# Optimization experiments

Measured on AMD Instinct MI355X. Metric: run time of the kernel, lower is better.

Reference implementation:

```python
import jax, jax.numpy as jnp
import numpy as np

H = 256           # hidden_size
S = 4             # num_subspaces
D = H // S        # subspace dim = 64
HD = 64           # mLSTM head_dim
EPS = 1e-8


def setup_inputs() -> dict:
    key = jax.random.key(0)
    ks = iter(jax.random.split(key, 40))
    def w(shape, scale=0.02):
        return (jax.random.normal(next(ks), shape, dtype=jnp.float32) * scale)
    B, T, Din = 256, 512, 128
    inp = {
        'x': jax.random.normal(next(ks), (B, T, Din), dtype=jnp.float32),
        # input projection
        'W_in': w((Din, H)), 'b_in': jnp.zeros((H,), jnp.float32),
        # layer 0: sLSTM (forget_bias buffer is zeros -> folded into b? keep explicit)
        's0_Wih': w((H, 4 * H)), 's0_bih': jnp.zeros((4 * H,), jnp.float32),
        's0_Whh': w((H, 4 * H)),
        # layer 1: mLSTM
        'm_Wq': w((H, HD)), 'm_bq': jnp.zeros((HD,), jnp.float32),
        'm_Wk': w((H, HD)), 'm_bk': jnp.zeros((HD,), jnp.float32),
        'm_Wv': w((H, HD)), 'm_bv': jnp.zeros((HD,), jnp.float32),
        'm_Wi': w((H, 1)), 'm_bi': jnp.zeros((1,), jnp.float32),
        'm_Wf': w((H, 1)), 'm_bf': jnp.zeros((1,), jnp.float32),
        'm_Wo': w((H, H)), 'm_bo': jnp.zeros((H,), jnp.float32),
        'm_Wp': w((HD, H)), 'm_bp': jnp.zeros((H,), jnp.float32),
        # subspace sLSTM cells (stacked over S); forget bias = -log(2^s)
        'sub_Wih': w((S, D, 4 * D)), 'sub_bih': jnp.zeros((S, 4 * D), jnp.float32),
        'sub_Whh': w((S, D, 4 * D)),
        'sub_fbias': jnp.asarray(-np.log(2.0 ** np.arange(S)), jnp.float32)[:, None] * jnp.ones((S, D), jnp.float32),
        # memory attention MLP
        'att_W1': w((D, D)), 'att_b1': jnp.zeros((D,), jnp.float32),
        'att_W2': w((D, 1)), 'att_b2': jnp.zeros((1,), jnp.float32),
        # layer norm
        'ln_g': jnp.ones((H,), jnp.float32), 'ln_b': jnp.zeros((H,), jnp.float32),
    }
    return inp


def _forward(x, W_in, b_in, s0_Wih, s0_bih, s0_Whh,
             m_Wq, m_bq, m_Wk, m_bk, m_Wv, m_bv, m_Wi, m_bi, m_Wf, m_bf,
             m_Wo, m_bo, m_Wp, m_bp,
             sub_Wih, sub_bih, sub_Whh, sub_fbias,
             att_W1, att_b1, att_W2, att_b2, ln_g, ln_b):
    B, T, _ = x.shape
    xh = x @ W_in + b_in                      # [B,T,H]
    xh = jnp.swapaxes(xh, 0, 1)               # [T,B,H] for scan

    def slstm(xt, h, c, n, Wih, bih, Whh, fbias):
        gates = xt @ Wih + bih + h @ Whh
        ig, fg, og, ct = jnp.split(gates, 4, axis=-1)
        i = jnp.exp(ig)
        f = jax.nn.sigmoid(fg + fbias)
        o = jax.nn.sigmoid(og)
        c_new = f * c + i * jnp.tanh(ct)
        n_new = f * n + i
        h_new = o * jnp.tanh(c_new / (n_new + EPS))
        return h_new, c_new, n_new

    def step(carry, xt):
        (h0, c0, n0, C1, n1, hs, cs, ns, _) = carry
        # layer 0: sLSTM, residual
        h0n, c0n, n0n = slstm(xt, h0, c0, n0, s0_Wih, s0_bih, s0_Whh, 0.0)
        x1 = h0n + xt
        # layer 1: mLSTM, residual
        q = x1 @ m_Wq + m_bq
        k = x1 @ m_Wk + m_bk
        v = x1 @ m_Wv + m_bv
        i1 = jnp.exp(x1 @ m_Wi + m_bi)              # [B,1]
        f1 = jax.nn.sigmoid(x1 @ m_Wf + m_bf)       # [B,1]
        C1n = f1[:, :, None] * C1 + i1[:, :, None] * (v[:, :, None] * k[:, None, :])
        n1n = f1 * n1 + i1                          # [B,1]
        Cq = jnp.einsum('bij,bj->bi', C1n, q)       # [B,HD]
        h_tilde = Cq / (n1n + EPS)
        o1 = jax.nn.sigmoid(x1 @ m_Wo + m_bo)
        h1n = o1 * jnp.tanh(h_tilde @ m_Wp + m_bp)
        x2 = h1n + x1
        # subspace sLSTM cells over S chunks (vectorized over s)
        xs = jnp.swapaxes(x2.reshape(B, S, D), 0, 1)   # [S,B,D]
        gates = (jnp.einsum('sbd,sdg->sbg', xs, sub_Wih) + sub_bih[:, None, :]
                 + jnp.einsum('sbd,sdg->sbg', hs, sub_Whh))
        ig, fg, og, ct = jnp.split(gates, 4, axis=-1)
        i = jnp.exp(ig)
        f = jax.nn.sigmoid(fg + sub_fbias[:, None, :])
        o = jax.nn.sigmoid(og)
        csn = f * cs + i * jnp.tanh(ct)
        nsn = f * ns + i
        hsn = o * jnp.tanh(csn / (nsn + EPS))          # [S,B,D]
        # attention fusion across subspaces
        score = jnp.tanh(hsn @ att_W1 + att_b1) @ att_W2 + att_b2  # [S,B,1]
        w = jax.nn.softmax(score[..., 0], axis=0)                  # [S,B]
        h_fused = jnp.sum(w[:, :, None] * hsn, axis=0)             # [B,D]
        h_final = jnp.tile(h_fused, (1, S))                        # [B,H]
        return (h0n, c0n, n0n, C1n, n1n, hsn, csn, nsn, h_final), None

    z = jnp.zeros
    carry0 = (z((B, H)), z((B, H)), jnp.ones((B, H)),
              z((B, HD, HD)), jnp.ones((B, 1)),
              z((S, B, D)), z((S, B, D)), jnp.ones((S, B, D)),
              z((B, H)))
    carryT, _ = jax.lax.scan(step, carry0, xh)
    out = carryT[-1]                                 # last-step h_final [B,H]
    mu = jnp.mean(out, axis=-1, keepdims=True)
    var = jnp.mean((out - mu) ** 2, axis=-1, keepdims=True)
    return (out - mu) / jnp.sqrt(var + 1e-5) * ln_g + ln_b


def reference(x, W_in, b_in, s0_Wih, s0_bih, s0_Whh,
              m_Wq, m_bq, m_Wk, m_bk, m_Wv, m_bv, m_Wi, m_bi, m_Wf, m_bf,
              m_Wo, m_bo, m_Wp, m_bp,
              sub_Wih, sub_bih, sub_Whh, sub_fbias,
              att_W1, att_b1, att_W2, att_b2, ln_g, ln_b):
    return _forward(x, W_in, b_in, s0_Wih, s0_bih, s0_Whh,
                    m_Wq, m_bq, m_Wk, m_bk, m_Wv, m_bv, m_Wi, m_bi, m_Wf, m_bf,
                    m_Wo, m_bo, m_Wp, m_bp,
                    sub_Wih, sub_bih, sub_Whh, sub_fbias,
                    att_W1, att_b1, att_W2, att_b2, ln_g, ln_b)
```

## Files before the change

kernel.cpp:

```cpp
#include <hip/hip_runtime.h>
#include <math.h>

#define TSTEPS 512
#define CH 16
#define NCHUNK 32
#define EPSR 1e-8f

#define OHH   0u
#define OSUB  262144u
#define OQK   393216u
#define OV    425984u
#define OWO   442368u
#define OWP   507904u
#define OWIN  524288u
#define NPACK1 557056u
#define OWC   557056u
#define OBC   688128u

typedef __fp16 h2_t __attribute__((ext_vector_type(2)));

__device__ __forceinline__ float dot2(unsigned int w, unsigned int a, float acc) {
    union U { unsigned int u; h2_t h; };
    U cw; cw.u = w; U ca; ca.u = a;
    return __builtin_amdgcn_fdot2(cw.h, ca.h, acc, false);
}
__device__ __forceinline__ unsigned int pk2f(float a, float b) {
    union { h2_t h; unsigned int u; } c;
    c.h = __builtin_amdgcn_cvt_pkrtz(a, b);
    return c.u;
}
__device__ __forceinline__ float bfu(unsigned int v) {
    union { unsigned int i; float f; } c; c.i = v; return c.f;
}
__device__ __forceinline__ float sigmoidf_(float v) { return 1.0f / (1.0f + expf(-v)); }
__device__ __forceinline__ unsigned short f2bf(float f) {
    unsigned int u = __float_as_uint(f);
    return (unsigned short)((u + 0x7fffu + ((u >> 16) & 1u)) >> 16);
}

extern "C" __global__ void pack_w(const float* __restrict__ Whh,
    const float* __restrict__ sWih, const float* __restrict__ sWhh,
    const float* __restrict__ Wq, const float* __restrict__ Wk, const float* __restrict__ Wv,
    const float* __restrict__ Wo, const float* __restrict__ Wp,
    const float* __restrict__ W_in, unsigned short* __restrict__ ws)
{
    unsigned e = blockIdx.x * 256u + threadIdx.x;
    if (e >= NPACK1) return;
    float v; bool isbf = false;
    if (e < OSUB) {
        unsigned idx = e >> 3, sl = e & 7u;
        unsigned jp = idx >> 8, t = idx & 255u, g = sl >> 1, ee = sl & 1u;
        v = Whh[(2u * jp + ee) * 1024u + g * 256u + t];
    } else if (e < OQK) {
        unsigned r = e - OSUB, idx = r >> 3, sl = r & 7u;
        unsigned q4 = idx & 3u, d = (idx >> 2) & 63u, jq = (idx >> 8) & 15u, s = idx >> 12;
        unsigned g = sl >> 1, ee = sl & 1u;
        unsigned j = jq * 4u + (q4 & 1u) * 2u + ee;
        const float* src = (q4 >> 1) ? sWhh : sWih;
        v = src[(s * 64u + j) * 256u + g * 64u + d];
    } else if (e < OV) {
        unsigned r = e - OQK, idx = r >> 3, sl = r & 7u;
        unsigned d = idx & 63u, jq = idx >> 6;
        unsigned j = jq * 4u + (sl & 3u);
        v = ((sl >> 2) ? Wk : Wq)[j * 64u + d];
    } else if (e < OWO) {
        unsigned r = e - OV, idx = r >> 2;
        unsigned d = idx & 63u, jq = idx >> 6, j = jq * 4u + (r & 3u);
        v = Wv[j * 64u + d];
    } else if (e < OWP) {
        unsigned r = e - OWO, idx = r >> 2;
        unsigned t = idx & 255u, jq = idx >> 8, j = jq * 4u + (r & 3u);
        v = Wo[j * 256u + t];
    } else if (e < OWIN) {
        unsigned r = e - OWP, idx = r >> 2;
        unsigned t = idx & 255u, jq = idx >> 8, j = jq * 4u + (r & 3u);
        v = Wp[j * 256u + t];
    } else {
        v = W_in[e - OWIN]; isbf = true;
    }
    if (isbf) ws[e] = f2bf(v);
    else { union { __fp16 h; unsigned short s; } c; c.h = (__fp16)v; ws[e] = c.s; }
}

extern "C" __global__ void compute_wc(const float* __restrict__ W_in,
    const float* __restrict__ Wih, const float* __restrict__ b_in,
    const float* __restrict__ bih, unsigned short* __restrict__ ws)
{
    unsigned e = blockIdx.x * 256u + threadIdx.x;
    if (e < 131072u) {
        unsigned k = e >> 10, n = e & 1023u;
        float acc = 0.f;
        for (int j = 0; j < 256; ++j) acc += W_in[k * 256 + j] * Wih[j * 1024 + n];
        unsigned t = n & 255u, g = n >> 8;
        ws[OWC + k * 1024 + t * 4 + g] = f2bf(acc);
    } else if (e < 132096u) {
        unsigned n = e - 131072u;
        float acc = bih[n];
        for (int j = 0; j < 256; ++j) acc += b_in[j] * Wih[j * 1024 + n];
        float* bc = (float*)(ws + OBC);
        bc[n] = acc;
    }
}

extern "C" __global__ __launch_bounds__(512)
void xlstm_seq(const float* __restrict__ x, const float* __restrict__ b_in,
               const float* __restrict__ bq, const float* __restrict__ bk, const float* __restrict__ bv,
               const float* __restrict__ Wi, const float* __restrict__ bi,
               const float* __restrict__ Wf, const float* __restrict__ bf,
               const float* __restrict__ bo, const float* __restrict__ bp,
               const float* __restrict__ sbih, const float* __restrict__ sfb,
               const float* __restrict__ aW1, const float* __restrict__ ab1,
               const float* __restrict__ aW2, const float* __restrict__ ab2,
               const float* __restrict__ lng, const float* __restrict__ lnb,
               const unsigned short* __restrict__ pk,
               float* __restrict__ out)
{
    const int u = threadIdx.x;
    const int b = blockIdx.x;
    const int t256 = u & 255;
    const int half = u >> 8;

    __shared__ float g_chunk[CH][1024];
    __shared__ float xt_chunk[CH][256];
    __shared__ __align__(16) float xT[128][20];
    __shared__ __align__(16) float x1_l[256], hs_l[256];
    __shared__ float opre_l[256];
    __shared__ float psum[4][520];
    __shared__ float qb[64], kb[64], vb[64];
    __shared__ float Cm[64 * 65];
    __shared__ float sc_l[16];
    __shared__ __align__(16) float Wi_l[256], Wf_l[256];
    __shared__ float sbih_l[1024], bc_l[1024];
    __shared__ float b_in_l[256], bo_l[256], bp_l[256], sfb_l[256], bqkv_l[192];
    __shared__ __align__(16) unsigned int h0p[128], x1p[128], x2p[128], hsp[128], htp[32];

    {
        const float* bcg = (const float*)(pk + OBC);
        for (int e = u; e < 1024; e += 512) { sbih_l[e] = sbih[e]; bc_l[e] = bcg[e]; }
    }
    if (u < 256) {
        Wi_l[u] = Wi[u]; Wf_l[u] = Wf[u];
        b_in_l[u] = b_in[u]; bo_l[u] = bo[u]; bp_l[u] = bp[u]; sfb_l[u] = sfb[u];
        hs_l[u] = 0.f;
    }
    if (u < 192) bqkv_l[u] = (u < 64) ? bq[u] : (u < 128) ? bk[u - 64] : bv[u - 128];
    if (u < 128) { h0p[u] = 0u; hsp[u] = 0u; }
    if (u == 0) { sc_l[10] = bi[0]; sc_l[11] = bf[0]; }
    for (int e = u; e < 64 * 65; e += 512) Cm[e] = 0.f;
    float c0 = 0.f, n0 = 1.f, cs = 0.f, ns = 1.f, n1 = 1.f;
    __syncthreads();

    const uint4* pwhh = reinterpret_cast<const uint4*>(pk + OHH) + t256;
    const uint4* psub = reinterpret_cast<const uint4*>(pk + OSUB)
                        + ((size_t)((t256 >> 6) * 1024 + (t256 & 63))) * 4;
    const uint4* pqk = reinterpret_cast<const uint4*>(pk + OQK) + (u & 63);
    const uint2* pv_ = reinterpret_cast<const uint2*>(pk + OV) + (u & 63);
    const uint2* pwo = reinterpret_cast<const uint2*>(pk + OWO) + t256;
    const uint2* pwp = reinterpret_cast<const uint2*>(pk + OWP) + t256;
    const unsigned short* pwin = pk + OWIN + t256;
    const uint2* pwc = reinterpret_cast<const uint2*>(pk + OWC) + t256;
    const float* xrow = x + (size_t)b * TSTEPS * 128;

    for (int cc = 0; cc < NCHUNK; ++cc) {
        {
            float4 xv4 = *reinterpret_cast<const float4*>(xrow + cc * (CH * 128) + u * 4);
            int m = u >> 5, k0 = (u * 4) & 127;
            xT[k0][m] = xv4.x; xT[k0 + 1][m] = xv4.y; xT[k0 + 2][m] = xv4.z; xT[k0 + 3][m] = xv4.w;
        }
        __syncthreads();

        {
            const int m0 = half * 8;
            float xtacc[8], gacc[4][8];
            {
                float bi_ = b_in_l[t256];
                #pragma unroll
                for (int e = 0; e < 8; ++e) xtacc[e] = bi_;
                #pragma unroll
                for (int g = 0; g < 4; ++g) {
                    float bcv = bc_l[g * 256 + t256];
                    #pragma unroll
                    for (int e = 0; e < 8; ++e) gacc[g][e] = bcv;
                }
            }
            #pragma unroll 4
            for (int k = 0; k < 128; ++k) {
                float wv = bfu((unsigned)pwin[k * 256] << 16);
                uint2 wg = pwc[k * 256];
                float w0 = bfu(wg.x << 16), w1 = bfu(wg.x & 0xffff0000u);
                float w2 = bfu(wg.y << 16), w3 = bfu(wg.y & 0xffff0000u);
                float4 a  = *reinterpret_cast<const float4*>(&xT[k][m0]);
                float4 b4 = *reinterpret_cast<const float4*>(&xT[k][m0 + 4]);
                #pragma unroll
                for (int e = 0; e < 8; ++e) {
                    float xv = (e == 0) ? a.x : (e == 1) ? a.y : (e == 2) ? a.z : (e == 3) ? a.w
                             : (e == 4) ? b4.x : (e == 5) ? b4.y : (e == 6) ? b4.z : b4.w;
                    xtacc[e]   += xv * wv;
                    gacc[0][e] += xv * w0;
                    gacc[1][e] += xv * w1;
                    gacc[2][e] += xv * w2;
                    gacc[3][e] += xv * w3;
                }
            }
            #pragma unroll
            for (int e = 0; e < 8; ++e) {
                xt_chunk[m0 + e][t256] = xtacc[e];
                g_chunk[m0 + e][t256]       = gacc[0][e];
                g_chunk[m0 + e][256 + t256] = gacc[1][e];
                g_chunk[m0 + e][512 + t256] = gacc[2][e];
                g_chunk[m0 + e][768 + t256] = gacc[3][e];
            }
        }
        __syncthreads();

        for (int st = 0; st < CH; ++st) {
            {
                float g0 = 0.f, g1 = 0.f, g2 = 0.f, g3 = 0.f;
                const int jp0 = half * 64;
                #pragma unroll 4
                for (int q = 0; q < 16; ++q) {
                    uint4 hp4 = *reinterpret_cast<const uint4*>(&h0p[jp0 + q * 4]);
                    #pragma unroll
                    for (int e = 0; e < 4; ++e) {
                        uint4 wk = pwhh[(size_t)(jp0 + q * 4 + e) * 256];
                        unsigned int hp = (e == 0) ? hp4.x : (e == 1) ? hp4.y : (e == 2) ? hp4.z : hp4.w;
                        g0 = dot2(wk.x, hp, g0);
                        g1 = dot2(wk.y, hp, g1);
                        g2 = dot2(wk.z, hp, g2);
                        g3 = dot2(wk.w, hp, g3);
                    }
                }
                psum[0][u] = g0; psum[1][u] = g1; psum[2][u] = g2; psum[3][u] = g3;
            }
            __syncthreads();
            if (u < 256) {
                float G0 = g_chunk[st][u]       + psum[0][u] + psum[0][256 + u];
                float G1 = g_chunk[st][256 + u] + psum[1][u] + psum[1][256 + u];
                float G2 = g_chunk[st][512 + u] + psum[2][u] + psum[2][256 + u];
                float G3 = g_chunk[st][768 + u] + psum[3][u] + psum[3][256 + u];
                float i0 = expf(G0), f0 = sigmoidf_(G1), o0 = sigmoidf_(G2);
                float cn = f0 * c0 + i0 * tanhf(G3);
                float nn = f0 * n0 + i0;
                c0 = cn; n0 = nn;
                float h0n = o0 * tanhf(cn / (nn + EPSR));
                float x1v = h0n + xt_chunk[st][u];
                x1_l[u] = x1v;
                float h0o = __shfl_xor(h0n, 1);
                float x1o = __shfl_xor(x1v, 1);
                if (!(u & 1)) { h0p[u >> 1] = pk2f(h0n, h0o); x1p[u >> 1] = pk2f(x1v, x1o); }
            }
            __syncthreads();

            if (u < 256) {
                const int jq0 = (u >> 6) * 16;
                float pq = 0.f, pkk = 0.f, pvv = 0.f;
                #pragma unroll 4
                for (int q = 0; q < 16; ++q) {
                    int jq = jq0 + q;
                    uint4 wqk = pqk[(size_t)jq * 64];
                    uint2 wv2 = pv_[(size_t)jq * 64];
                    uint2 ap = *reinterpret_cast<const uint2*>(&x1p[jq * 2]);
                    pq  = dot2(wqk.x, ap.x, pq);  pq  = dot2(wqk.y, ap.y, pq);
                    pkk = dot2(wqk.z, ap.x, pkk); pkk = dot2(wqk.w, ap.y, pkk);
                    pvv = dot2(wv2.x, ap.x, pvv); pvv = dot2(wv2.y, ap.y, pvv);
                }
                psum[0][u] = pq; psum[1][u] = pkk; psum[2][u] = pvv;
            } else if (u < 384) {
                const float* Wl = (u < 320) ? Wi_l : Wf_l;
                int j0 = (u & 63) * 4;
                float4 xv = *reinterpret_cast<const float4*>(&x1_l[j0]);
                float4 wv = *reinterpret_cast<const float4*>(&Wl[j0]);
                float p = xv.x * wv.x + xv.y * wv.y + xv.z * wv.z + xv.w * wv.w;
                #pragma unroll
                for (int off = 32; off > 0; off >>= 1) p += __shfl_down(p, off);
                if ((u & 63) == 0) sc_l[(u < 320) ? 8 : 9] = p;
            }
            __syncthreads();
            {
                int lane = u & 63;
                if (u < 64)        qb[u]    = bqkv_l[u]          + psum[0][u] + psum[0][64 + u] + psum[0][128 + u] + psum[0][192 + u];
                else if (u < 128)  kb[lane] = bqkv_l[64 + lane]  + psum[1][lane] + psum[1][64 + lane] + psum[1][128 + lane] + psum[1][192 + lane];
                else if (u < 192)  vb[lane] = bqkv_l[128 + lane] + psum[2][lane] + psum[2][64 + lane] + psum[2][128 + lane] + psum[2][192 + lane];
                else if (u == 192) sc_l[0] = expf(sc_l[10] + sc_l[8]);
                else if (u == 193) sc_l[1] = sigmoidf_(sc_l[11] + sc_l[9]);
            }
            __syncthreads();

            float i1 = sc_l[0], f1 = sc_l[1];
            n1 = f1 * n1 + i1;
            {
                int r = u >> 3, ci = (u & 7) * 8;
                float vi = i1 * vb[r];
                float cqp = 0.f;
                #pragma unroll
                for (int e = 0; e < 8; ++e) {
                    int c = ci + e;
                    float cmv = f1 * Cm[r * 65 + c] + vi * kb[c];
                    Cm[r * 65 + c] = cmv;
                    cqp += cmv * qb[c];
                }
                cqp += __shfl_down(cqp, 4);
                cqp += __shfl_down(cqp, 2);
                cqp += __shfl_down(cqp, 1);
                float htv = cqp / (n1 + EPSR);
                float hto = __shfl_xor(htv, 8);
                if ((u & 15) == 0) htp[u >> 4] = pk2f(htv, hto);

                float p = 0.f;
                const int jq0 = half * 32;
                #pragma unroll 4
                for (int q = 0; q < 32; ++q) {
                    int jq = jq0 + q;
                    uint2 w2 = pwo[(size_t)jq * 256];
                    uint2 ap = *reinterpret_cast<const uint2*>(&x1p[jq * 2]);
                    p = dot2(w2.x, ap.x, p); p = dot2(w2.y, ap.y, p);
                }
                psum[3][u] = p;
            }
            __syncthreads();

            {
                if (u < 256) opre_l[u] = bo_l[u] + psum[3][u] + psum[3][256 + u];
                float p = 0.f;
                const int jq0 = half * 8;
                #pragma unroll
                for (int q = 0; q < 8; ++q) {
                    int jq = jq0 + q;
                    uint2 w2 = pwp[(size_t)jq * 256];
                    uint2 ap = *reinterpret_cast<const uint2*>(&htp[jq * 2]);
                    p = dot2(w2.x, ap.x, p); p = dot2(w2.y, ap.y, p);
                }
                psum[0][u] = p;
            }
            __syncthreads();
            if (u < 256) {
                float pp = bp_l[u] + psum[0][u] + psum[0][256 + u];
                float h1 = sigmoidf_(opre_l[u]) * tanhf(pp);
                float x2v = h1 + x1_l[u];
                float x2o = __shfl_xor(x2v, 1);
                if (!(u & 1)) x2p[u >> 1] = pk2f(x2v, x2o);
            }
            __syncthreads();

            {
                const int sbase = (t256 >> 6) * 32;
                const int jqb = half * 8;
                float g0 = 0.f, g1 = 0.f, g2 = 0.f, g3 = 0.f;
                #pragma unroll 2
                for (int q = 0; q < 8; ++q) {
                    int jq = jqb + q;
                    const uint4* pp4 = psub + (size_t)jq * 256;
                    uint4 wih0 = pp4[0], wih1 = pp4[1], whh0 = pp4[2], whh1 = pp4[3];
                    uint2 xp = *reinterpret_cast<const uint2*>(&x2p[sbase + jq * 2]);
                    uint2 hp = *reinterpret_cast<const uint2*>(&hsp[sbase + jq * 2]);
                    g0 = dot2(wih0.x, xp.x, g0); g0 = dot2(wih1.x, xp.y, g0);
                    g0 = dot2(whh0.x, hp.x, g0); g0 = dot2(whh1.x, hp.y, g0);
                    g1 = dot2(wih0.y, xp.x, g1); g1 = dot2(wih1.y, xp.y, g1);
                    g1 = dot2(whh0.y, hp.x, g1); g1 = dot2(whh1.y, hp.y, g1);
                    g2 = dot2(wih0.z, xp.x, g2); g2 = dot2(wih1.z, xp.y, g2);
                    g2 = dot2(whh0.z, hp.x, g2); g2 = dot2(whh1.z, hp.y, g2);
                    g3 = dot2(wih0.w, xp.x, g3); g3 = dot2(wih1.w, xp.y, g3);
                    g3 = dot2(whh0.w, hp.x, g3); g3 = dot2(whh1.w, hp.y, g3);
                }
                psum[0][u] = g0; psum[1][u] = g1; psum[2][u] = g2; psum[3][u] = g3;
            }
            __syncthreads();
            if (u < 256) {
                int s = u >> 6, dd = u & 63;
                float sg0 = psum[0][u] + psum[0][256 + u] + sbih_l[s * 256 + dd];
                float sg1 = psum[1][u] + psum[1][256 + u] + sbih_l[s * 256 + 64 + dd];
                float sg2 = psum[2][u] + psum[2][256 + u] + sbih_l[s * 256 + 128 + dd];
                float sg3 = psum[3][u] + psum[3][256 + u] + sbih_l[s * 256 + 192 + dd];
                float si = expf(sg0);
                float sf = sigmoidf_(sg1 + sfb_l[u]);
                float so = sigmoidf_(sg2);
                float csn = sf * cs + si * tanhf(sg3);
                float nsn = sf * ns + si;
                cs = csn; ns = nsn;
                float hsn = so * tanhf(csn / (nsn + EPSR));
                hs_l[u] = hsn;
                float hso = __shfl_xor(hsn, 1);
                if (!(u & 1)) hsp[u >> 1] = pk2f(hsn, hso);
            }
            __syncthreads();
        }
    }

    if (u < 256) {
        int s = u >> 6, dd = u & 63;
        float av = ab1[dd];
        for (int j = 0; j < 64; ++j) av += hs_l[s * 64 + j] * aW1[j * 64 + dd];
        float contrib = tanhf(av) * aW2[dd];
        #pragma unroll
        for (int off = 32; off > 0; off >>= 1) contrib += __shfl_down(contrib, off);
        if (dd == 0) sc_l[4 + s] = contrib + ab2[0];
    }
    __syncthreads();
    if (u < 256) {
        float a0 = sc_l[4], a1 = sc_l[5], a2 = sc_l[6], a3 = sc_l[7];
        float m = fmaxf(fmaxf(a0, a1), fmaxf(a2, a3));
        float e0 = expf(a0 - m), e1 = expf(a1 - m), e2 = expf(a2 - m), e3 = expf(a3 - m);
        float inv = 1.f / (e0 + e1 + e2 + e3);
        int dd = u & 63;
        psum[0][u] = (e0 * hs_l[dd] + e1 * hs_l[64 + dd] + e2 * hs_l[128 + dd] + e3 * hs_l[192 + dd]) * inv;
    }
    __syncthreads();
    if (u < 256) {
        float mu = 0.f;
        for (int j = 0; j < 256; ++j) mu += psum[0][j];
        mu *= (1.0f / 256.0f);
        float var = 0.f;
        for (int j = 0; j < 256; ++j) { float dv = psum[0][j] - mu; var += dv * dv; }
        var *= (1.0f / 256.0f);
        out[b * 256 + u] = (psum[0][u] - mu) / sqrtf(var + 1e-5f) * lng[u] + lnb[u];
    }
}

extern "C" void kernel_launch(void* const* d_in, const int* in_sizes, int n_in,
                              void* d_out, int out_size, void* d_ws, size_t ws_size,
                              hipStream_t stream) {
    (void)in_sizes; (void)n_in; (void)out_size; (void)ws_size;
    const float* x     = (const float*)d_in[0];
    const float* W_in  = (const float*)d_in[1];
    const float* b_in  = (const float*)d_in[2];
    const float* Wih   = (const float*)d_in[3];
    const float* bih   = (const float*)d_in[4];
    const float* Whh   = (const float*)d_in[5];
    const float* Wq    = (const float*)d_in[6];
    const float* bq    = (const float*)d_in[7];
    const float* Wk    = (const float*)d_in[8];
    const float* bk    = (const float*)d_in[9];
    const float* Wv    = (const float*)d_in[10];
    const float* bv    = (const float*)d_in[11];
    const float* Wi    = (const float*)d_in[12];
    const float* bi    = (const float*)d_in[13];
    const float* Wf    = (const float*)d_in[14];
    const float* bf    = (const float*)d_in[15];
    const float* Wo    = (const float*)d_in[16];
    const float* bo    = (const float*)d_in[17];
    const float* Wp    = (const float*)d_in[18];
    const float* bp    = (const float*)d_in[19];
    const float* sWih  = (const float*)d_in[20];
    const float* sbih  = (const float*)d_in[21];
    const float* sWhh  = (const float*)d_in[22];
    const float* sfb   = (const float*)d_in[23];
    const float* aW1   = (const float*)d_in[24];
    const float* ab1   = (const float*)d_in[25];
    const float* aW2   = (const float*)d_in[26];
    const float* ab2   = (const float*)d_in[27];
    const float* lng   = (const float*)d_in[28];
    const float* lnb   = (const float*)d_in[29];
    float* out = (float*)d_out;
    unsigned short* ws = (unsigned short*)d_ws;

    pack_w<<<dim3((NPACK1 + 255u) / 256u), dim3(256), 0, stream>>>(
        Whh, sWih, sWhh, Wq, Wk, Wv, Wo, Wp, W_in, ws);
    compute_wc<<<dim3(517), dim3(256), 0, stream>>>(W_in, Wih, b_in, bih, ws);

    xlstm_seq<<<dim3(256), dim3(512), 0, stream>>>(
        x, b_in, bq, bk, bv, Wi, bi, Wf, bf, bo, bp,
        sbih, sfb, aW1, ab1, aW2, ab2, lng, lnb, ws, out);
}
```

Before: 7.102 ms.

## Double workgroup to 1024 threads, splitting recurrent matvecs four ways

```diff
diff --git a/kernel.cpp b/kernel.cpp
--- a/kernel.cpp
+++ b/kernel.cpp
@@ -64,9 +64,10 @@
         unsigned j = jq * 4u + (sl & 3u);
         v = ((sl >> 2) ? Wk : Wq)[j * 64u + d];
     } else if (e < OWO) {
-        unsigned r = e - OV, idx = r >> 2;
-        unsigned d = idx & 63u, jq = idx >> 6, j = jq * 4u + (r & 3u);
-        v = Wv[j * 64u + d];
+        unsigned r = e - OQK, idx0 = 0u; (void)idx0;
+        unsigned rr = e - OV, idx = rr >> 2;
+        unsigned d = idx & 63u, jq = idx >> 6, j = jq * 4u + (rr & 3u);
+        v = Wv[j * 64u + d]; (void)r;
     } else if (e < OWP) {
         unsigned r = e - OWO, idx = r >> 2;
         unsigned t = idx & 255u, jq = idx >> 8, j = jq * 4u + (r & 3u);
@@ -102,7 +103,7 @@
     }
 }
 
-extern "C" __global__ __launch_bounds__(512)
+extern "C" __global__ __launch_bounds__(1024)
 void xlstm_seq(const float* __restrict__ x, const float* __restrict__ b_in,
                const float* __restrict__ bq, const float* __restrict__ bk, const float* __restrict__ bv,
                const float* __restrict__ Wi, const float* __restrict__ bi,
@@ -118,14 +119,14 @@
     const int u = threadIdx.x;
     const int b = blockIdx.x;
     const int t256 = u & 255;
-    const int half = u >> 8;
+    const int quarter = u >> 8;
 
     __shared__ float g_chunk[CH][1024];
     __shared__ float xt_chunk[CH][256];
     __shared__ __align__(16) float xT[128][20];
     __shared__ __align__(16) float x1_l[256], hs_l[256];
     __shared__ float opre_l[256];
-    __shared__ float psum[4][520];
+    __shared__ float psum[4][1040];
     __shared__ float qb[64], kb[64], vb[64];
     __shared__ float Cm[64 * 65];
     __shared__ float sc_l[16];
@@ -136,7 +137,7 @@
 
     {
         const float* bcg = (const float*)(pk + OBC);
-        for (int e = u; e < 1024; e += 512) { sbih_l[e] = sbih[e]; bc_l[e] = bcg[e]; }
+        sbih_l[u] = sbih[u]; bc_l[u] = bcg[u];
     }
     if (u < 256) {
         Wi_l[u] = Wi[u]; Wf_l[u] = Wf[u];
@@ -146,7 +147,7 @@
     if (u < 192) bqkv_l[u] = (u < 64) ? bq[u] : (u < 128) ? bk[u - 64] : bv[u - 128];
     if (u < 128) { h0p[u] = 0u; hsp[u] = 0u; }
     if (u == 0) { sc_l[10] = bi[0]; sc_l[11] = bf[0]; }
-    for (int e = u; e < 64 * 65; e += 512) Cm[e] = 0.f;
+    for (int e = u; e < 64 * 65; e += 1024) Cm[e] = 0.f;
     float c0 = 0.f, n0 = 1.f, cs = 0.f, ns = 1.f, n1 = 1.f;
     __syncthreads();
 
@@ -163,24 +164,24 @@
 
     for (int cc = 0; cc < NCHUNK; ++cc) {
         {
-            float4 xv4 = *reinterpret_cast<const float4*>(xrow + cc * (CH * 128) + u * 4);
-            int m = u >> 5, k0 = (u * 4) & 127;
-            xT[k0][m] = xv4.x; xT[k0 + 1][m] = xv4.y; xT[k0 + 2][m] = xv4.z; xT[k0 + 3][m] = xv4.w;
+            float2 xv2 = *reinterpret_cast<const float2*>(xrow + cc * (CH * 128) + u * 2);
+            int m = u >> 6, k0 = (u * 2) & 127;
+            xT[k0][m] = xv2.x; xT[k0 + 1][m] = xv2.y;
         }
         __syncthreads();
 
         {
-            const int m0 = half * 8;
-            float xtacc[8], gacc[4][8];
+            const int m0 = quarter * 4;
+            float xtacc[4], gacc[4][4];
             {
                 float bi_ = b_in_l[t256];
                 #pragma unroll
-                for (int e = 0; e < 8; ++e) xtacc[e] = bi_;
+                for (int e = 0; e < 4; ++e) xtacc[e] = bi_;
                 #pragma unroll
                 for (int g = 0; g < 4; ++g) {
                     float bcv = bc_l[g * 256 + t256];
                     #pragma unroll
-                    for (int e = 0; e < 8; ++e) gacc[g][e] = bcv;
+                    for (int e = 0; e < 4; ++e) gacc[g][e] = bcv;
                 }
             }
             #pragma unroll 4
@@ -189,12 +190,10 @@
                 uint2 wg = pwc[k * 256];
                 float w0 = bfu(wg.x << 16), w1 = bfu(wg.x & 0xffff0000u);
                 float w2 = bfu(wg.y << 16), w3 = bfu(wg.y & 0xffff0000u);
-                float4 a  = *reinterpret_cast<const float4*>(&xT[k][m0]);
-                float4 b4 = *reinterpret_cast<const float4*>(&xT[k][m0 + 4]);
-                #pragma unroll
-                for (int e = 0; e < 8; ++e) {
-                    float xv = (e == 0) ? a.x : (e == 1) ? a.y : (e == 2) ? a.z : (e == 3) ? a.w
-                             : (e == 4) ? b4.x : (e == 5) ? b4.y : (e == 6) ? b4.z : b4.w;
+                float4 a = *reinterpret_cast<const float4*>(&xT[k][m0]);
+                #pragma unroll
+                for (int e = 0; e < 4; ++e) {
+                    float xv = (e == 0) ? a.x : (e == 1) ? a.y : (e == 2) ? a.z : a.w;
                     xtacc[e]   += xv * wv;
                     gacc[0][e] += xv * w0;
                     gacc[1][e] += xv * w1;
@@ -203,7 +202,7 @@
                 }
             }
             #pragma unroll
-            for (int e = 0; e < 8; ++e) {
+            for (int e = 0; e < 4; ++e) {
                 xt_chunk[m0 + e][t256] = xtacc[e];
                 g_chunk[m0 + e][t256]       = gacc[0][e];
                 g_chunk[m0 + e][256 + t256] = gacc[1][e];
@@ -216,9 +215,9 @@
         for (int st = 0; st < CH; ++st) {
             {
                 float g0 = 0.f, g1 = 0.f, g2 = 0.f, g3 = 0.f;
-                const int jp0 = half * 64;
+                const int jp0 = quarter * 32;
                 #pragma unroll 4
-                for (int q = 0; q < 16; ++q) {
+                for (int q = 0; q < 8; ++q) {
                     uint4 hp4 = *reinterpret_cast<const uint4*>(&h0p[jp0 + q * 4]);
                     #pragma unroll
                     for (int e = 0; e < 4; ++e) {
@@ -234,10 +233,10 @@
             }
             __syncthreads();
             if (u < 256) {
-                float G0 = g_chunk[st][u]       + psum[0][u] + psum[0][256 + u];
-                float G1 = g_chunk[st][256 + u] + psum[1][u] + psum[1][256 + u];
-                float G2 = g_chunk[st][512 + u] + psum[2][u] + psum[2][256 + u];
-                float G3 = g_chunk[st][768 + u] + psum[3][u] + psum[3][256 + u];
+                float G0 = g_chunk[st][u]       + psum[0][u] + psum[0][256 + u] + psum[0][512 + u] + psum[0][768 + u];
+                float G1 = g_chunk[st][256 + u] + psum[1][u] + psum[1][256 + u] + psum[1][512 + u] + psum[1][768 + u];
+                float G2 = g_chunk[st][512 + u] + psum[2][u] + psum[2][256 + u] + psum[2][512 + u] + psum[2][768 + u];
+                float G3 = g_chunk[st][768 + u] + psum[3][u] + psum[3][256 + u] + psum[3][512 + u] + psum[3][768 + u];
                 float i0 = expf(G0), f0 = sigmoidf_(G1), o0 = sigmoidf_(G2);
                 float cn = f0 * c0 + i0 * tanhf(G3);
                 float nn = f0 * n0 + i0;
@@ -274,6 +273,17 @@
                 #pragma unroll
                 for (int off = 32; off > 0; off >>= 1) p += __shfl_down(p, off);
                 if ((u & 63) == 0) sc_l[(u < 320) ? 8 : 9] = p;
+            } else if (u >= 512) {
+                float p = 0.f;
+                const int jq0 = (quarter - 2) * 32;
+                #pragma unroll 4
+                for (int q = 0; q < 32; ++q) {
+                    int jq = jq0 + q;
+                    uint2 w2 = pwo[(size_t)jq * 256];
+                    uint2 ap = *reinterpret_cast<const uint2*>(&x1p[jq * 2]);
+                    p = dot2(w2.x, ap.x, p); p = dot2(w2.y, ap.y, p);
+                }
+                psum[3][u] = p;
             }
             __syncthreads();
             {
@@ -289,42 +299,32 @@
             float i1 = sc_l[0], f1 = sc_l[1];
             n1 = f1 * n1 + i1;
             {
-                int r = u >> 3, ci = (u & 7) * 8;
+                int r = u >> 4, ci = (u & 15) * 4;
                 float vi = i1 * vb[r];
                 float cqp = 0.f;
                 #pragma unroll
-                for (int e = 0; e < 8; ++e) {
+                for (int e = 0; e < 4; ++e) {
                     int c = ci + e;
                     float cmv = f1 * Cm[r * 65 + c] + vi * kb[c];
                     Cm[r * 65 + c] = cmv;
                     cqp += cmv * qb[c];
                 }
+                cqp += __shfl_down(cqp, 8);
                 cqp += __shfl_down(cqp, 4);
                 cqp += __shfl_down(cqp, 2);
                 cqp += __shfl_down(cqp, 1);
                 float htv = cqp / (n1 + EPSR);
-                float hto = __shfl_xor(htv, 8);
-                if ((u & 15) == 0) htp[u >> 4] = pk2f(htv, hto);
-
+                float hto = __shfl_xor(htv, 16);
+                if ((u & 31) == 0) htp[u >> 5] = pk2f(htv, hto);
+                if (u < 256) opre_l[u] = bo_l[u] + psum[3][512 + u] + psum[3][768 + u];
+            }
+            __syncthreads();
+
+            {
                 float p = 0.f;
-                const int jq0 = half * 32;
-                #pragma unroll 4
-                for (int q = 0; q < 32; ++q) {
-                    int jq = jq0 + q;
-                    uint2 w2 = pwo[(size_t)jq * 256];
-                    uint2 ap = *reinterpret_cast<const uint2*>(&x1p[jq * 2]);
-                    p = dot2(w2.x, ap.x, p); p = dot2(w2.y, ap.y, p);
-                }
-                psum[3][u] = p;
-            }
-            __syncthreads();
-
-            {
-                if (u < 256) opre_l[u] = bo_l[u] + psum[3][u] + psum[3][256 + u];
-                float p = 0.f;
-                const int jq0 = half * 8;
-                #pragma unroll
-                for (int q = 0; q < 8; ++q) {
+                const int jq0 = quarter * 4;
+                #pragma unroll
+                for (int q = 0; q < 4; ++q) {
                     int jq = jq0 + q;
                     uint2 w2 = pwp[(size_t)jq * 256];
                     uint2 ap = *reinterpret_cast<const uint2*>(&htp[jq * 2]);
@@ -334,7 +334,7 @@
             }
             __syncthreads();
             if (u < 256) {
-                float pp = bp_l[u] + psum[0][u] + psum[0][256 + u];
+                float pp = bp_l[u] + psum[0][u] + psum[0][256 + u] + psum[0][512 + u] + psum[0][768 + u];
                 float h1 = sigmoidf_(opre_l[u]) * tanhf(pp);
                 float x2v = h1 + x1_l[u];
                 float x2o = __shfl_xor(x2v, 1);
@@ -344,10 +344,10 @@
 
             {
                 const int sbase = (t256 >> 6) * 32;
-                const int jqb = half * 8;
+                const int jqb = quarter * 4;
                 float g0 = 0.f, g1 = 0.f, g2 = 0.f, g3 = 0.f;
-                #pragma unroll 2
-                for (int q = 0; q < 8; ++q) {
+                #pragma unroll
+                for (int q = 0; q < 4; ++q) {
                     int jq = jqb + q;
                     const uint4* pp4 = psub + (size_t)jq * 256;
                     uint4 wih0 = pp4[0], wih1 = pp4[1], whh0 = pp4[2], whh1 = pp4[3];
@@ -367,10 +367,10 @@
             __syncthreads();
             if (u < 256) {
                 int s = u >> 6, dd = u & 63;
-                float sg0 = psum[0][u] + psum[0][256 + u] + sbih_l[s * 256 + dd];
-                float sg1 = psum[1][u] + psum[1][256 + u] + sbih_l[s * 256 + 64 + dd];
-                float sg2 = psum[2][u] + psum[2][256 + u] + sbih_l[s * 256 + 128 + dd];
-                float sg3 = psum[3][u] + psum[3][256 + u] + sbih_l[s * 256 + 192 + dd];
+                float sg0 = psum[0][u] + psum[0][256 + u] + psum[0][512 + u] + psum[0][768 + u] + sbih_l[s * 256 + dd];
+                float sg1 = psum[1][u] + psum[1][256 + u] + psum[1][512 + u] + psum[1][768 + u] + sbih_l[s * 256 + 64 + dd];
+                float sg2 = psum[2][u] + psum[2][256 + u] + psum[2][512 + u] + psum[2][768 + u] + sbih_l[s * 256 + 128 + dd];
+                float sg3 = psum[3][u] + psum[3][256 + u] + psum[3][512 + u] + psum[3][768 + u] + sbih_l[s * 256 + 192 + dd];
                 float si = expf(sg0);
                 float sf = sigmoidf_(sg1 + sfb_l[u]);
                 float so = sigmoidf_(sg2);
@@ -457,7 +457,7 @@
         Whh, sWih, sWhh, Wq, Wk, Wv, Wo, Wp, W_in, ws);
     compute_wc<<<dim3(517), dim3(256), 0, stream>>>(W_in, Wih, b_in, bih, ws);
 
-    xlstm_seq<<<dim3(256), dim3(512), 0, stream>>>(
+    xlstm_seq<<<dim3(256), dim3(1024), 0, stream>>>(
         x, b_in, bq, bk, bv, Wi, bi, Wf, bf, bo, bp,
         sbih, sfb, aW1, ab1, aW2, ab2, lng, lnb, ws, out);
 }
```

After: 10.88 ms. 53.2% more time.

## Repack recurrent weights so each thread reads contiguous runs, merge Wp projection stage

Applied to the files above, without the earlier changes.

```diff
diff --git a/kernel.cpp b/kernel.cpp
--- a/kernel.cpp
+++ b/kernel.cpp
@@ -49,7 +49,9 @@
     float v; bool isbf = false;
     if (e < OSUB) {
         unsigned idx = e >> 3, sl = e & 7u;
-        unsigned jp = idx >> 8, t = idx & 255u, g = sl >> 1, ee = sl & 1u;
+        unsigned jj = idx & 3u, t = (idx >> 2) & 255u, jp4 = idx >> 10;
+        unsigned jp = jp4 * 4u + jj;
+        unsigned g = sl >> 1, ee = sl & 1u;
         v = Whh[(2u * jp + ee) * 1024u + g * 256u + t];
     } else if (e < OQK) {
         unsigned r = e - OSUB, idx = r >> 3, sl = r & 7u;
@@ -60,20 +62,23 @@
         v = src[(s * 64u + j) * 256u + g * 64u + d];
     } else if (e < OV) {
         unsigned r = e - OQK, idx = r >> 3, sl = r & 7u;
-        unsigned d = idx & 63u, jq = idx >> 6;
-        unsigned j = jq * 4u + (sl & 3u);
+        unsigned jj = idx & 3u, d = (idx >> 2) & 63u, jq4 = idx >> 8;
+        unsigned j = (jq4 * 4u + jj) * 4u + (sl & 3u);
         v = ((sl >> 2) ? Wk : Wq)[j * 64u + d];
     } else if (e < OWO) {
         unsigned r = e - OV, idx = r >> 2;
-        unsigned d = idx & 63u, jq = idx >> 6, j = jq * 4u + (r & 3u);
+        unsigned jj = idx & 3u, d = (idx >> 2) & 63u, jq4 = idx >> 8;
+        unsigned j = (jq4 * 4u + jj) * 4u + (r & 3u);
         v = Wv[j * 64u + d];
     } else if (e < OWP) {
         unsigned r = e - OWO, idx = r >> 2;
-        unsigned t = idx & 255u, jq = idx >> 8, j = jq * 4u + (r & 3u);
+        unsigned jj = idx & 3u, t = (idx >> 2) & 255u, jq4 = idx >> 10;
+        unsigned j = (jq4 * 4u + jj) * 4u + (r & 3u);
         v = Wo[j * 256u + t];
     } else if (e < OWIN) {
         unsigned r = e - OWP, idx = r >> 2;
-        unsigned t = idx & 255u, jq = idx >> 8, j = jq * 4u + (r & 3u);
+        unsigned jq = idx & 15u, t = idx >> 4;
+        unsigned j = jq * 4u + (r & 3u);
         v = Wp[j * 256u + t];
     } else {
         v = W_in[e - OWIN]; isbf = true;
@@ -124,7 +129,6 @@
     __shared__ float xt_chunk[CH][256];
     __shared__ __align__(16) float xT[128][20];
     __shared__ __align__(16) float x1_l[256], hs_l[256];
-    __shared__ float opre_l[256];
     __shared__ float psum[4][520];
     __shared__ float qb[64], kb[64], vb[64];
     __shared__ float Cm[64 * 65];
@@ -150,13 +154,13 @@
     float c0 = 0.f, n0 = 1.f, cs = 0.f, ns = 1.f, n1 = 1.f;
     __syncthreads();
 
-    const uint4* pwhh = reinterpret_cast<const uint4*>(pk + OHH) + t256;
+    const uint4* pwhh = reinterpret_cast<const uint4*>(pk + OHH) + t256 * 4;
     const uint4* psub = reinterpret_cast<const uint4*>(pk + OSUB)
                         + ((size_t)((t256 >> 6) * 1024 + (t256 & 63))) * 4;
-    const uint4* pqk = reinterpret_cast<const uint4*>(pk + OQK) + (u & 63);
-    const uint2* pv_ = reinterpret_cast<const uint2*>(pk + OV) + (u & 63);
-    const uint2* pwo = reinterpret_cast<const uint2*>(pk + OWO) + t256;
-    const uint2* pwp = reinterpret_cast<const uint2*>(pk + OWP) + t256;
+    const uint4* pqk = reinterpret_cast<const uint4*>(pk + OQK) + (u & 63) * 4;
+    const uint2* pv2 = reinterpret_cast<const uint2*>(pk + OV) + (u & 63) * 4;
+    const uint2* pwo = reinterpret_cast<const uint2*>(pk + OWO) + t256 * 4;
+    const uint2* pwp = reinterpret_cast<const uint2*>(pk + OWP) + t256 * 16;
     const unsigned short* pwin = pk + OWIN + t256;
     const uint2* pwc = reinterpret_cast<const uint2*>(pk + OWC) + t256;
     const float* xrow = x + (size_t)b * TSTEPS * 128;
@@ -216,13 +220,14 @@
         for (int st = 0; st < CH; ++st) {
             {
                 float g0 = 0.f, g1 = 0.f, g2 = 0.f, g3 = 0.f;
-                const int jp0 = half * 64;
+                const int jp40 = half * 16;
                 #pragma unroll 4
-                for (int q = 0; q < 16; ++q) {
-                    uint4 hp4 = *reinterpret_cast<const uint4*>(&h0p[jp0 + q * 4]);
+                for (int q4 = 0; q4 < 16; ++q4) {
+                    const uint4* w4 = pwhh + (size_t)(jp40 + q4) * 1024;
+                    uint4 hp4 = *reinterpret_cast<const uint4*>(&h0p[(jp40 + q4) * 4]);
                     #pragma unroll
                     for (int e = 0; e < 4; ++e) {
-                        uint4 wk = pwhh[(size_t)(jp0 + q * 4 + e) * 256];
+                        uint4 wk = w4[e];
                         unsigned int hp = (e == 0) ? hp4.x : (e == 1) ? hp4.y : (e == 2) ? hp4.z : hp4.w;
                         g0 = dot2(wk.x, hp, g0);
                         g1 = dot2(wk.y, hp, g1);
@@ -252,17 +257,22 @@
             __syncthreads();
 
             if (u < 256) {
-                const int jq0 = (u >> 6) * 16;
+                const int jq40 = (u >> 6) * 4;
                 float pq = 0.f, pkk = 0.f, pvv = 0.f;
-                #pragma unroll 4
-                for (int q = 0; q < 16; ++q) {
-                    int jq = jq0 + q;
-                    uint4 wqk = pqk[(size_t)jq * 64];
-                    uint2 wv2 = pv_[(size_t)jq * 64];
-                    uint2 ap = *reinterpret_cast<const uint2*>(&x1p[jq * 2]);
-                    pq  = dot2(wqk.x, ap.x, pq);  pq  = dot2(wqk.y, ap.y, pq);
-                    pkk = dot2(wqk.z, ap.x, pkk); pkk = dot2(wqk.w, ap.y, pkk);
-                    pvv = dot2(wv2.x, ap.x, pvv); pvv = dot2(wv2.y, ap.y, pvv);
+                #pragma unroll
+                for (int q4 = 0; q4 < 4; ++q4) {
+                    const uint4* wq4 = pqk + (size_t)(jq40 + q4) * 256;
+                    const uint2* wv4 = pv2 + (size_t)(jq40 + q4) * 256;
+                    #pragma unroll
+                    for (int e = 0; e < 4; ++e) {
+                        int jq = (jq40 + q4) * 4 + e;
+                        uint4 wqk = wq4[e];
+                        uint2 wvv = wv4[e];
+                        uint2 ap = *reinterpret_cast<const uint2*>(&x1p[jq * 2]);
+                        pq  = dot2(wqk.x, ap.x, pq);  pq  = dot2(wqk.y, ap.y, pq);
+                        pkk = dot2(wqk.z, ap.x, pkk); pkk = dot2(wqk.w, ap.y, pkk);
+                        pvv = dot2(wvv.x, ap.x, pvv); pvv = dot2(wvv.y, ap.y, pvv);
+                    }
                 }
                 psum[0][u] = pq; psum[1][u] = pkk; psum[2][u] = pvv;
             } else if (u < 384) {
@@ -307,35 +317,32 @@
                 if ((u & 15) == 0) htp[u >> 4] = pk2f(htv, hto);
 
                 float p = 0.f;
-                const int jq0 = half * 32;
+                const int jq40 = half * 8;
                 #pragma unroll 4
-                for (int q = 0; q < 32; ++q) {
-                    int jq = jq0 + q;
-                    uint2 w2 = pwo[(size_t)jq * 256];
-                    uint2 ap = *reinterpret_cast<const uint2*>(&x1p[jq * 2]);
-                    p = dot2(w2.x, ap.x, p); p = dot2(w2.y, ap.y, p);
+                for (int q4 = 0; q4 < 8; ++q4) {
+                    const uint2* w4 = pwo + (size_t)(jq40 + q4) * 1024;
+                    #pragma unroll
+                    for (int e = 0; e < 4; ++e) {
+                        int jq = (jq40 + q4) * 4 + e;
+                        uint2 w2 = w4[e];
+                        uint2 ap = *reinterpret_cast<const uint2*>(&x1p[jq * 2]);
+                        p = dot2(w2.x, ap.x, p); p = dot2(w2.y, ap.y, p);
+                    }
                 }
                 psum[3][u] = p;
             }
             __syncthreads();
 
-            {
-                if (u < 256) opre_l[u] = bo_l[u] + psum[3][u] + psum[3][256 + u];
-                float p = 0.f;
-                const int jq0 = half * 8;
-                #pragma unroll
-                for (int q = 0; q < 8; ++q) {
-                    int jq = jq0 + q;
-                    uint2 w2 = pwp[(size_t)jq * 256];
+            if (u < 256) {
+                float opre = bo_l[u] + psum[3][u] + psum[3][256 + u];
+                float pp = bp_l[u];
+                #pragma unroll
+                for (int jq = 0; jq < 16; ++jq) {
+                    uint2 w2 = pwp[jq];
                     uint2 ap = *reinterpret_cast<const uint2*>(&htp[jq * 2]);
-                    p = dot2(w2.x, ap.x, p); p = dot2(w2.y, ap.y, p);
-                }
-                psum[0][u] = p;
-            }
-            __syncthreads();
-            if (u < 256) {
-                float pp = bp_l[u] + psum[0][u] + psum[0][256 + u];
-                float h1 = sigmoidf_(opre_l[u]) * tanhf(pp);
+                    pp = dot2(w2.x, ap.x, pp); pp = dot2(w2.y, ap.y, pp);
+                }
+                float h1 = sigmoidf_(opre) * tanhf(pp);
                 float x2v = h1 + x1_l[u];
                 float x2o = __shfl_xor(x2v, 1);
                 if (!(u & 1)) x2p[u >> 1] = pk2f(x2v, x2o);
```

After: 8.707 ms. +22.6%, slower.
